# Kernel tuning notes

Measured on AMD Instinct MI355X. Metric: run time of the kernel, lower is better.

Reference implementation:

```python
import jax, jax.numpy as jnp
import numpy as np

N_NODES = 100000
N_EDGES = 1600000
Z_DIM = 64
EDGE_FEAT_DIM = 16
HIDDEN = 128


def setup_inputs() -> dict:
    key = jax.random.key(0)
    k_z, k_ei, k_ea, k_w1, k_b1, k_w2, k_b2 = jax.random.split(key, 7)
    in_dim = 2 * Z_DIM + EDGE_FEAT_DIM
    return {
        "z": jax.random.normal(k_z, (N_NODES, Z_DIM), dtype=jnp.float32),
        "edge_index": jax.random.randint(k_ei, (2, N_EDGES), 0, N_NODES, dtype=jnp.int64),
        "edge_attr": jax.random.normal(k_ea, (N_EDGES, EDGE_FEAT_DIM), dtype=jnp.float32),
        # decoder_mlp params: Linear(2*z_dim+edge_feat_dim, 128) -> ReLU -> Linear(128, 1)
        "W1": jax.random.normal(k_w1, (in_dim, HIDDEN), dtype=jnp.float32) / np.float32(np.sqrt(in_dim)),
        "b1": jax.random.normal(k_b1, (HIDDEN,), dtype=jnp.float32) * 0.01,
        "W2": jax.random.normal(k_w2, (HIDDEN, 1), dtype=jnp.float32) / np.float32(np.sqrt(HIDDEN)),
        "b2": jax.random.normal(k_b2, (1,), dtype=jnp.float32) * 0.01,
    }


def reference(z, edge_index, edge_attr, W1, b1, W2, b2):
    # decode(): gather endpoint embeddings, concat edge features, 2-layer MLP, sigmoid
    src = edge_index[0]
    dst = edge_index[1]
    edge_input = jnp.concatenate([z[src], z[dst], edge_attr], axis=1)  # [E, 2Z+F]
    h = jax.nn.relu(edge_input @ W1 + b1)  # [E, 128]
    logits = h @ W2 + b2                   # [E, 1]
    return jax.nn.sigmoid(logits).squeeze(-1)  # [E]
```

## Files before the change

kernel.cpp:

```cpp
#include <hip/hip_runtime.h>

#define EDGES 1600000
#define NN    100000
#define ZD    64
#define FD    16
#define HID   128
#define BM    32
#define THREADS 256
#define NBLK  1250
#define TPW   10
#define NFRAG 2560
#define WT_SHORTS (NFRAG * 8)

typedef __attribute__((ext_vector_type(8)))  short bfrag;
typedef __attribute__((ext_vector_type(16))) float f16v;

__device__ __forceinline__ unsigned short f2bf(float f) {
  unsigned u = __builtin_bit_cast(unsigned, f);
  u += 0x7fffu + ((u >> 16) & 1u);
  return (unsigned short)(u >> 16);
}
__device__ __forceinline__ unsigned cvtpk(float lo, float hi) {
  unsigned r;
  asm("v_cvt_pk_bf16_f32 %0, %1, %2" : "=v"(r) : "v"(lo), "v"(hi));
  return r;
}
__device__ __forceinline__ void gload16(const void* g, void* l) {
  __builtin_amdgcn_global_load_lds(
      (const __attribute__((address_space(1))) unsigned int*)g,
      (__attribute__((address_space(3))) unsigned int*)l, 16, 0, 0);
}

__global__ void zconv_kernel(const float* __restrict__ z,
                             unsigned short* __restrict__ z16, int n4) {
  int i = blockIdx.x * blockDim.x + threadIdx.x;
  if (i >= n4) return;
  float4 f = reinterpret_cast<const float4*>(z)[i];
  ushort4 p;
  p.x = f2bf(f.x); p.y = f2bf(f.y); p.z = f2bf(f.z); p.w = f2bf(f.w);
  reinterpret_cast<ushort4*>(z16)[i] = p;
}

__global__ void wtab_kernel(const float* __restrict__ W1,
                            const float* __restrict__ b1,
                            unsigned short* __restrict__ WT) {
  int i = blockIdx.x * blockDim.x + threadIdx.x;
  if (i >= WT_SHORTS) return;
  int j    = i & 7;
  int frag = i >> 3;
  int lane = frag & 63;
  int s    = (frag >> 6) % 10;
  int blk  = frag / 640;
  int hid  = blk * 32 + (lane & 31);
  int k    = s * 16 + (lane >> 5) * 8 + j;
  float v = (k < 144) ? W1[k * HID + hid] : (k == 144 ? b1[hid] : 0.f);
  WT[i] = f2bf(v);
}

template<bool ZB>
__global__ __launch_bounds__(THREADS, 2) void fused_kernel(
    const float* __restrict__ zf, const unsigned short* __restrict__ z16,
    const unsigned short* __restrict__ WT,
    const int* __restrict__ ei, const float* __restrict__ ea,
    const float* __restrict__ W2, const float* __restrict__ b2,
    float* __restrict__ out)
{
  __shared__ __align__(16) int4 sW[NFRAG];

  const int tid  = threadIdx.x;
  const int lane = tid & 63;
  const int wid  = tid >> 6;
  const int e    = lane & 31;
  const int hi   = lane >> 5;

  #pragma unroll
  for (int c = 0; c < 10; ++c)
    gload16(WT + (size_t)(c * 256 + tid) * 8, &sW[c * 256 + tid]);
  asm volatile("s_waitcnt vmcnt(0)" ::: "memory");
  __syncthreads();

  float w2v[64];
  #pragma unroll
  for (int blk = 0; blk < 4; ++blk)
    #pragma unroll
    for (int rg = 0; rg < 16; ++rg) {
      int rh = (rg & 3) + 8 * (rg >> 2) + 4 * hi;
      w2v[blk * 16 + rg] = W2[blk * 32 + rh];
    }
  const float bias2 = b2[0];

  int4 oq = {0, 0, 0, 0};
  if (hi == 0) oq.x = 0x3F80;
  const bfrag cone = __builtin_bit_cast(bfrag, oq);

#define GZ(x0, x1, x2, x3, x4, x5, x6, x7, x8, si, di, tt) do {                \
    if constexpr (ZB) {                                                        \
      const unsigned short* ps_ = z16 + (size_t)(si) * ZD + hi * 8;            \
      const unsigned short* pd_ = z16 + (size_t)(di) * ZD + hi * 8;            \
      x0 = *reinterpret_cast<const bfrag*>(ps_);                               \
      x1 = *reinterpret_cast<const bfrag*>(ps_ + 16);                          \
      x2 = *reinterpret_cast<const bfrag*>(ps_ + 32);                          \
      x3 = *reinterpret_cast<const bfrag*>(ps_ + 48);                          \
      x4 = *reinterpret_cast<const bfrag*>(pd_);                               \
      x5 = *reinterpret_cast<const bfrag*>(pd_ + 16);                          \
      x6 = *reinterpret_cast<const bfrag*>(pd_ + 32);                          \
      x7 = *reinterpret_cast<const bfrag*>(pd_ + 48);                          \
    } else {                                                                   \
      const float* ps_ = zf + (size_t)(si) * ZD + hi * 8;                      \
      const float* pd_ = zf + (size_t)(di) * ZD + hi * 8;                      \
      float4 a_, b_;                                                           \
      a_ = ((const float4*)ps_)[0]; b_ = ((const float4*)ps_)[1];              \
      { int4 q_ = {(int)cvtpk(a_.x,a_.y),(int)cvtpk(a_.z,a_.w),                \
                   (int)cvtpk(b_.x,b_.y),(int)cvtpk(b_.z,b_.w)};               \
        x0 = __builtin_bit_cast(bfrag, q_); }                                  \
      a_ = ((const float4*)(ps_+16))[0]; b_ = ((const float4*)(ps_+16))[1];    \
      { int4 q_ = {(int)cvtpk(a_.x,a_.y),(int)cvtpk(a_.z,a_.w),                \
                   (int)cvtpk(b_.x,b_.y),(int)cvtpk(b_.z,b_.w)};               \
        x1 = __builtin_bit_cast(bfrag, q_); }                                  \
      a_ = ((const float4*)(ps_+32))[0]; b_ = ((const float4*)(ps_+32))[1];    \
      { int4 q_ = {(int)cvtpk(a_.x,a_.y),(int)cvtpk(a_.z,a_.w),                \
                   (int)cvtpk(b_.x,b_.y),(int)cvtpk(b_.z,b_.w)};               \
        x2 = __builtin_bit_cast(bfrag, q_); }                                  \
      a_ = ((const float4*)(ps_+48))[0]; b_ = ((const float4*)(ps_+48))[1];    \
      { int4 q_ = {(int)cvtpk(a_.x,a_.y),(int)cvtpk(a_.z,a_.w),                \
                   (int)cvtpk(b_.x,b_.y),(int)cvtpk(b_.z,b_.w)};               \
        x3 = __builtin_bit_cast(bfrag, q_); }                                  \
      a_ = ((const float4*)pd_)[0]; b_ = ((const float4*)pd_)[1];              \
      { int4 q_ = {(int)cvtpk(a_.x,a_.y),(int)cvtpk(a_.z,a_.w),                \
                   (int)cvtpk(b_.x,b_.y),(int)cvtpk(b_.z,b_.w)};               \
        x4 = __builtin_bit_cast(bfrag, q_); }                                  \
      a_ = ((const float4*)(pd_+16))[0]; b_ = ((const float4*)(pd_+16))[1];    \
      { int4 q_ = {(int)cvtpk(a_.x,a_.y),(int)cvtpk(a_.z,a_.w),                \
                   (int)cvtpk(b_.x,b_.y),(int)cvtpk(b_.z,b_.w)};               \
        x5 = __builtin_bit_cast(bfrag, q_); }                                  \
      a_ = ((const float4*)(pd_+32))[0]; b_ = ((const float4*)(pd_+32))[1];    \
      { int4 q_ = {(int)cvtpk(a_.x,a_.y),(int)cvtpk(a_.z,a_.w),                \
                   (int)cvtpk(b_.x,b_.y),(int)cvtpk(b_.z,b_.w)};               \
        x6 = __builtin_bit_cast(bfrag, q_); }                                  \
      a_ = ((const float4*)(pd_+48))[0]; b_ = ((const float4*)(pd_+48))[1];    \
      { int4 q_ = {(int)cvtpk(a_.x,a_.y),(int)cvtpk(a_.z,a_.w),                \
                   (int)cvtpk(b_.x,b_.y),(int)cvtpk(b_.z,b_.w)};               \
        x7 = __builtin_bit_cast(bfrag, q_); }                                  \
    }                                                                          \
    const float* pe_ = ea + ((size_t)(tt) * BM + e) * FD + hi * 8;             \
    float4 ea_ = ((const float4*)pe_)[0];                                      \
    float4 eb_ = ((const float4*)pe_)[1];                                      \
    { int4 q_ = {(int)cvtpk(ea_.x,ea_.y),(int)cvtpk(ea_.z,ea_.w),              \
                 (int)cvtpk(eb_.x,eb_.y),(int)cvtpk(eb_.z,eb_.w)};             \
      x8 = __builtin_bit_cast(bfrag, q_); }                                    \
  } while (0)

  const int gw = blockIdx.x * 4 + wid;
  const int T0 = gw * TPW;

  int si = ei[(size_t)T0 * BM + e];
  int di = ei[(size_t)EDGES + (size_t)T0 * BM + e];
  bfrag c0, c1, c2, c3, c4, c5, c6, c7, c8;
  GZ(c0, c1, c2, c3, c4, c5, c6, c7, c8, si, di, T0);
  int s1 = ei[(size_t)(T0 + 1) * BM + e];
  int d1 = ei[(size_t)EDGES + (size_t)(T0 + 1) * BM + e];

  for (int t = 0; t < TPW; ++t) {
    const int tt = T0 + t;

    const int tn = (t + 1 < TPW) ? tt + 1 : tt;
    bfrag n0, n1, n2, n3, n4, n5, n6, n7, n8;
    GZ(n0, n1, n2, n3, n4, n5, n6, n7, n8, s1, d1, tn);

    const int tf = (t + 2 < TPW) ? tt + 2 : T0 + TPW - 1;
    s1 = ei[(size_t)tf * BM + e];
    d1 = ei[(size_t)EDGES + (size_t)tf * BM + e];

    float p = 0.f;
    #pragma unroll
    for (int blk = 0; blk < 4; ++blk) {
      const int4* wp = &sW[blk * 640 + lane];
      bfrag w0 = *reinterpret_cast<const bfrag*>(wp + 0 * 64);
      bfrag w1 = *reinterpret_cast<const bfrag*>(wp + 1 * 64);
      bfrag w2 = *reinterpret_cast<const bfrag*>(wp + 2 * 64);
      bfrag w3 = *reinterpret_cast<const bfrag*>(wp + 3 * 64);
      bfrag w4 = *reinterpret_cast<const bfrag*>(wp + 4 * 64);
      bfrag w5 = *reinterpret_cast<const bfrag*>(wp + 5 * 64);
      bfrag w6 = *reinterpret_cast<const bfrag*>(wp + 6 * 64);
      bfrag w7 = *reinterpret_cast<const bfrag*>(wp + 7 * 64);
      bfrag w8 = *reinterpret_cast<const bfrag*>(wp + 8 * 64);
      bfrag w9 = *reinterpret_cast<const bfrag*>(wp + 9 * 64);

      f16v acc;
      #pragma unroll
      for (int rg = 0; rg < 16; ++rg) acc[rg] = 0.f;
      acc = __builtin_amdgcn_mfma_f32_32x32x16_bf16(w0, c0, acc, 0, 0, 0);
      acc = __builtin_amdgcn_mfma_f32_32x32x16_bf16(w1, c1, acc, 0, 0, 0);
      acc = __builtin_amdgcn_mfma_f32_32x32x16_bf16(w2, c2, acc, 0, 0, 0);
      acc = __builtin_amdgcn_mfma_f32_32x32x16_bf16(w3, c3, acc, 0, 0, 0);
      acc = __builtin_amdgcn_mfma_f32_32x32x16_bf16(w4, c4, acc, 0, 0, 0);
      acc = __builtin_amdgcn_mfma_f32_32x32x16_bf16(w5, c5, acc, 0, 0, 0);
      acc = __builtin_amdgcn_mfma_f32_32x32x16_bf16(w6, c6, acc, 0, 0, 0);
      acc = __builtin_amdgcn_mfma_f32_32x32x16_bf16(w7, c7, acc, 0, 0, 0);
      acc = __builtin_amdgcn_mfma_f32_32x32x16_bf16(w8, c8, acc, 0, 0, 0);
      acc = __builtin_amdgcn_mfma_f32_32x32x16_bf16(w9, cone, acc, 0, 0, 0);

      #pragma unroll
      for (int rg = 0; rg < 16; ++rg)
        p = fmaf(fmaxf(acc[rg], 0.f), w2v[blk * 16 + rg], p);
    }

    p += __shfl_xor(p, 32);
    if (lane < 32)
      out[(size_t)tt * BM + lane] = 1.f / (1.f + __expf(-(p + bias2)));

    c0 = n0; c1 = n1; c2 = n2; c3 = n3; c4 = n4;
    c5 = n5; c6 = n6; c7 = n7; c8 = n8;
  }
#undef GZ
}

extern "C" void kernel_launch(void* const* d_in, const int* in_sizes, int n_in,
                              void* d_out, int out_size, void* d_ws, size_t ws_size,
                              hipStream_t stream) {
  const float* z  = (const float*)d_in[0];
  const int*   ei = (const int*)d_in[1];
  const float* ea = (const float*)d_in[2];
  const float* W1 = (const float*)d_in[3];
  const float* b1 = (const float*)d_in[4];
  const float* W2 = (const float*)d_in[5];
  const float* b2 = (const float*)d_in[6];
  float* out = (float*)d_out;

  const size_t z16_bytes = (size_t)NN * ZD * sizeof(unsigned short);
  const size_t wt_bytes  = (size_t)WT_SHORTS * sizeof(unsigned short);

  if (ws_size >= z16_bytes + wt_bytes) {
    unsigned short* z16 = (unsigned short*)d_ws;
    unsigned short* WT  = z16 + (size_t)NN * ZD;
    const int n4 = NN * ZD / 4;
    zconv_kernel<<<(n4 + 255) / 256, 256, 0, stream>>>(z, z16, n4);
    wtab_kernel<<<(WT_SHORTS + 255) / 256, 256, 0, stream>>>(W1, b1, WT);
    fused_kernel<true><<<NBLK, THREADS, 0, stream>>>(
        z, z16, WT, ei, ea, W2, b2, out);
  } else {
    unsigned short* WT = (unsigned short*)d_ws;
    wtab_kernel<<<(WT_SHORTS + 255) / 256, 256, 0, stream>>>(W1, b1, WT);
    fused_kernel<false><<<NBLK, THREADS, 0, stream>>>(
        z, nullptr, WT, ei, ea, W2, b2, out);
  }
}
```

Baseline: 99.31 us.

## Split MFMA chain into two accumulators, move W2 to LDS, halve tiles per wave

The single dependent chain of ten MFMAs becomes two independent chains of five, so the matrix unit can interleave them. The partial sums are added before ReLU, and the W2 dot product now uses four accumulators. W2 moves from a 64-float register array into LDS to cut register pressure, and each block now handles half as many tiles, which doubles the block count. In exchange the kernel does an extra vector add per element and more LDS reads, and the per-block weight staging into LDS is repeated twice as often.

```diff
diff --git a/kernel.cpp b/kernel.cpp
--- a/kernel.cpp
+++ b/kernel.cpp
@@ -7,8 +7,8 @@
 #define HID   128
 #define BM    32
 #define THREADS 256
-#define NBLK  1250
-#define TPW   10
+#define NBLK  2500
+#define TPW   5
 #define NFRAG 2560
 #define WT_SHORTS (NFRAG * 8)
 
@@ -66,6 +66,7 @@
     float* __restrict__ out)
 {
   __shared__ __align__(16) int4 sW[NFRAG];
+  __shared__ __align__(16) float sW2[HID];
 
   const int tid  = threadIdx.x;
   const int lane = tid & 63;
@@ -76,22 +77,19 @@
   #pragma unroll
   for (int c = 0; c < 10; ++c)
     gload16(WT + (size_t)(c * 256 + tid) * 8, &sW[c * 256 + tid]);
+  if (tid < HID) sW2[tid] = W2[tid];
   asm volatile("s_waitcnt vmcnt(0)" ::: "memory");
   __syncthreads();
 
-  float w2v[64];
-  #pragma unroll
-  for (int blk = 0; blk < 4; ++blk)
-    #pragma unroll
-    for (int rg = 0; rg < 16; ++rg) {
-      int rh = (rg & 3) + 8 * (rg >> 2) + 4 * hi;
-      w2v[blk * 16 + rg] = W2[blk * 32 + rh];
-    }
   const float bias2 = b2[0];
 
   int4 oq = {0, 0, 0, 0};
   if (hi == 0) oq.x = 0x3F80;
   const bfrag cone = __builtin_bit_cast(bfrag, oq);
+
+  f16v zerov;
+  #pragma unroll
+  for (int rg = 0; rg < 16; ++rg) zerov[rg] = 0.f;
 
 #define GZ(x0, x1, x2, x3, x4, x5, x6, x7, x8, si, di, tt) do {                \
     if constexpr (ZB) {                                                        \
@@ -171,40 +169,60 @@
     s1 = ei[(size_t)tf * BM + e];
     d1 = ei[(size_t)EDGES + (size_t)tf * BM + e];
 
-    float p = 0.f;
+    float p0 = 0.f, p1 = 0.f, p2 = 0.f, p3 = 0.f;
     #pragma unroll
     for (int blk = 0; blk < 4; ++blk) {
       const int4* wp = &sW[blk * 640 + lane];
+
       bfrag w0 = *reinterpret_cast<const bfrag*>(wp + 0 * 64);
+      bfrag w2 = *reinterpret_cast<const bfrag*>(wp + 2 * 64);
+      bfrag w4 = *reinterpret_cast<const bfrag*>(wp + 4 * 64);
+      bfrag w6 = *reinterpret_cast<const bfrag*>(wp + 6 * 64);
+      bfrag w8 = *reinterpret_cast<const bfrag*>(wp + 8 * 64);
+      f16v accA;
+      accA = __builtin_amdgcn_mfma_f32_32x32x16_bf16(w0, c0, zerov, 0, 0, 0);
+      accA = __builtin_amdgcn_mfma_f32_32x32x16_bf16(w2, c2, accA, 0, 0, 0);
+      accA = __builtin_amdgcn_mfma_f32_32x32x16_bf16(w4, c4, accA, 0, 0, 0);
+      accA = __builtin_amdgcn_mfma_f32_32x32x16_bf16(w6, c6, accA, 0, 0, 0);
+      accA = __builtin_amdgcn_mfma_f32_32x32x16_bf16(w8, c8, accA, 0, 0, 0);
+
+      bfrag w9 = *reinterpret_cast<const bfrag*>(wp + 9 * 64);
       bfrag w1 = *reinterpret_cast<const bfrag*>(wp + 1 * 64);
-      bfrag w2 = *reinterpret_cast<const bfrag*>(wp + 2 * 64);
       bfrag w3 = *reinterpret_cast<const bfrag*>(wp + 3 * 64);
-      bfrag w4 = *reinterpret_cast<const bfrag*>(wp + 4 * 64);
       bfrag w5 = *reinterpret_cast<const bfrag*>(wp + 5 * 64);
-      bfrag w6 = *reinterpret_cast<const bfrag*>(wp + 6 * 64);
       bfrag w7 = *reinterpret_cast<const bfrag*>(wp + 7 * 64);
-      bfrag w8 = *reinterpret_cast<const bfrag*>(wp + 8 * 64);
-      bfrag w9 = *reinterpret_cast<const bfrag*>(wp + 9 * 64);
-
-      f16v acc;
-      #pragma unroll
-      for (int rg = 0; rg < 16; ++rg) acc[rg] = 0.f;
-      acc = __builtin_amdgcn_mfma_f32_32x32x16_bf16(w0, c0, acc, 0, 0, 0);
-      acc = __builtin_amdgcn_mfma_f32_32x32x16_bf16(w1, c1, acc, 0, 0, 0);
-      acc = __builtin_amdgcn_mfma_f32_32x32x16_bf16(w2, c2, acc, 0, 0, 0);
-      acc = __builtin_amdgcn_mfma_f32_32x32x16_bf16(w3, c3, acc, 0, 0, 0);
-      acc = __builtin_amdgcn_mfma_f32_32x32x16_bf16(w4, c4, acc, 0, 0, 0);
-      acc = __builtin_amdgcn_mfma_f32_32x32x16_bf16(w5, c5, acc, 0, 0, 0);
-      acc = __builtin_amdgcn_mfma_f32_32x32x16_bf16(w6, c6, acc, 0, 0, 0);
-      acc = __builtin_amdgcn_mfma_f32_32x32x16_bf16(w7, c7, acc, 0, 0, 0);
-      acc = __builtin_amdgcn_mfma_f32_32x32x16_bf16(w8, c8, acc, 0, 0, 0);
-      acc = __builtin_amdgcn_mfma_f32_32x32x16_bf16(w9, cone, acc, 0, 0, 0);
-
-      #pragma unroll
-      for (int rg = 0; rg < 16; ++rg)
-        p = fmaf(fmaxf(acc[rg], 0.f), w2v[blk * 16 + rg], p);
+      f16v accB;
+      accB = __builtin_amdgcn_mfma_f32_32x32x16_bf16(w9, cone, zerov, 0, 0, 0);
+      accB = __builtin_amdgcn_mfma_f32_32x32x16_bf16(w1, c1, accB, 0, 0, 0);
+      accB = __builtin_amdgcn_mfma_f32_32x32x16_bf16(w3, c3, accB, 0, 0, 0);
+      accB = __builtin_amdgcn_mfma_f32_32x32x16_bf16(w5, c5, accB, 0, 0, 0);
+      accB = __builtin_amdgcn_mfma_f32_32x32x16_bf16(w7, c7, accB, 0, 0, 0);
+
+      const float* wq = &sW2[blk * 32 + 4 * hi];
+      float4 q0 = *reinterpret_cast<const float4*>(wq);
+      float4 q1 = *reinterpret_cast<const float4*>(wq + 8);
+      float4 q2 = *reinterpret_cast<const float4*>(wq + 16);
+      float4 q3 = *reinterpret_cast<const float4*>(wq + 24);
+
+      p0 = fmaf(fmaxf(accA[0]  + accB[0],  0.f), q0.x, p0);
+      p1 = fmaf(fmaxf(accA[1]  + accB[1],  0.f), q0.y, p1);
+      p2 = fmaf(fmaxf(accA[2]  + accB[2],  0.f), q0.z, p2);
+      p3 = fmaf(fmaxf(accA[3]  + accB[3],  0.f), q0.w, p3);
+      p0 = fmaf(fmaxf(accA[4]  + accB[4],  0.f), q1.x, p0);
+      p1 = fmaf(fmaxf(accA[5]  + accB[5],  0.f), q1.y, p1);
+      p2 = fmaf(fmaxf(accA[6]  + accB[6],  0.f), q1.z, p2);
+      p3 = fmaf(fmaxf(accA[7]  + accB[7],  0.f), q1.w, p3);
+      p0 = fmaf(fmaxf(accA[8]  + accB[8],  0.f), q2.x, p0);
+      p1 = fmaf(fmaxf(accA[9]  + accB[9],  0.f), q2.y, p1);
+      p2 = fmaf(fmaxf(accA[10] + accB[10], 0.f), q2.z, p2);
+      p3 = fmaf(fmaxf(accA[11] + accB[11], 0.f), q2.w, p3);
+      p0 = fmaf(fmaxf(accA[12] + accB[12], 0.f), q3.x, p0);
+      p1 = fmaf(fmaxf(accA[13] + accB[13], 0.f), q3.y, p1);
+      p2 = fmaf(fmaxf(accA[14] + accB[14], 0.f), q3.z, p2);
+      p3 = fmaf(fmaxf(accA[15] + accB[15], 0.f), q3.w, p3);
     }
 
+    float p = (p0 + p1) + (p2 + p3);
     p += __shfl_xor(p, 32);
     if (lane < 32)
       out[(size_t)tt * BM + lane] = 1.f / (1.f + __expf(-(p + bias2)));
```

New measurement: 107.9 us. 8.7% more time.

## Deepen gather prefetch, split MFMA chains, move W2 to LDS, raise occupancy

Applied to the files above, without the earlier changes.

Each wave now handles 5 tiles instead of 10, with twice as many blocks. The loop is fully unrolled into a triple-buffered schedule that keeps two tiles of gathers in flight ahead of compute. The per-tile MFMA chain is split into two independent accumulators to shorten the dependency chain. W2 moves from 64 per-thread registers into shared memory, freeing registers so launch bounds can ask for 3 blocks per SM. The cost is more LDS reads for W2, more prologue work (the weight-table load into LDS) per edge handled, and register pressure from the three live buffers.

```diff
diff --git a/kernel.cpp b/kernel.cpp
--- a/kernel.cpp
+++ b/kernel.cpp
@@ -7,8 +7,8 @@
 #define HID   128
 #define BM    32
 #define THREADS 256
-#define NBLK  1250
-#define TPW   10
+#define NBLK  2500
+#define TPW   5
 #define NFRAG 2560
 #define WT_SHORTS (NFRAG * 8)
 
@@ -58,7 +58,7 @@
 }
 
 template<bool ZB>
-__global__ __launch_bounds__(THREADS, 2) void fused_kernel(
+__global__ __launch_bounds__(THREADS, 3) void fused_kernel(
     const float* __restrict__ zf, const unsigned short* __restrict__ z16,
     const unsigned short* __restrict__ WT,
     const int* __restrict__ ei, const float* __restrict__ ea,
@@ -66,6 +66,7 @@
     float* __restrict__ out)
 {
   __shared__ __align__(16) int4 sW[NFRAG];
+  __shared__ __align__(16) float sW2[HID];
 
   const int tid  = threadIdx.x;
   const int lane = tid & 63;
@@ -76,24 +77,21 @@
   #pragma unroll
   for (int c = 0; c < 10; ++c)
     gload16(WT + (size_t)(c * 256 + tid) * 8, &sW[c * 256 + tid]);
+  if (tid < HID) sW2[tid] = W2[tid];
   asm volatile("s_waitcnt vmcnt(0)" ::: "memory");
   __syncthreads();
 
-  float w2v[64];
-  #pragma unroll
-  for (int blk = 0; blk < 4; ++blk)
-    #pragma unroll
-    for (int rg = 0; rg < 16; ++rg) {
-      int rh = (rg & 3) + 8 * (rg >> 2) + 4 * hi;
-      w2v[blk * 16 + rg] = W2[blk * 32 + rh];
-    }
   const float bias2 = b2[0];
 
   int4 oq = {0, 0, 0, 0};
   if (hi == 0) oq.x = 0x3F80;
   const bfrag cone = __builtin_bit_cast(bfrag, oq);
 
-#define GZ(x0, x1, x2, x3, x4, x5, x6, x7, x8, si, di, tt) do {                \
+  f16v zerov;
+  #pragma unroll
+  for (int rg = 0; rg < 16; ++rg) zerov[rg] = 0.f;
+
+#define GZ(x0, x1, x2, x3, x4, x5, x6, x7, xa, xb, si, di, tt) do {            \
     if constexpr (ZB) {                                                        \
       const unsigned short* ps_ = z16 + (size_t)(si) * ZD + hi * 8;            \
       const unsigned short* pd_ = z16 + (size_t)(di) * ZD + hi * 8;            \
@@ -143,76 +141,99 @@
         x7 = __builtin_bit_cast(bfrag, q_); }                                  \
     }                                                                          \
     const float* pe_ = ea + ((size_t)(tt) * BM + e) * FD + hi * 8;             \
-    float4 ea_ = ((const float4*)pe_)[0];                                      \
-    float4 eb_ = ((const float4*)pe_)[1];                                      \
-    { int4 q_ = {(int)cvtpk(ea_.x,ea_.y),(int)cvtpk(ea_.z,ea_.w),              \
-                 (int)cvtpk(eb_.x,eb_.y),(int)cvtpk(eb_.z,eb_.w)};             \
-      x8 = __builtin_bit_cast(bfrag, q_); }                                    \
+    xa = ((const float4*)pe_)[0];                                              \
+    xb = ((const float4*)pe_)[1];                                              \
+  } while (0)
+
+#define COMPUTE(x0, x1, x2, x3, x4, x5, x6, x7, xa, xb, tt) do {               \
+    int4 eq_ = {(int)cvtpk(xa.x, xa.y), (int)cvtpk(xa.z, xa.w),                \
+                (int)cvtpk(xb.x, xb.y), (int)cvtpk(xb.z, xb.w)};               \
+    bfrag x8 = __builtin_bit_cast(bfrag, eq_);                                 \
+    float p0 = 0.f, p1 = 0.f, p2 = 0.f, p3 = 0.f;                              \
+    _Pragma("unroll")                                                          \
+    for (int blk = 0; blk < 4; ++blk) {                                        \
+      const int4* wp = &sW[blk * 640 + lane];                                  \
+      bfrag w0 = *reinterpret_cast<const bfrag*>(wp + 0 * 64);                 \
+      bfrag w2 = *reinterpret_cast<const bfrag*>(wp + 2 * 64);                 \
+      bfrag w4 = *reinterpret_cast<const bfrag*>(wp + 4 * 64);                 \
+      bfrag w6 = *reinterpret_cast<const bfrag*>(wp + 6 * 64);                 \
+      bfrag w8 = *reinterpret_cast<const bfrag*>(wp + 8 * 64);                 \
+      f16v accA;                                                               \
+      accA = __builtin_amdgcn_mfma_f32_32x32x16_bf16(w0, x0, zerov, 0, 0, 0);  \
+      accA = __builtin_amdgcn_mfma_f32_32x32x16_bf16(w2, x2, accA, 0, 0, 0);   \
+      accA = __builtin_amdgcn_mfma_f32_32x32x16_bf16(w4, x4, accA, 0, 0, 0);   \
+      accA = __builtin_amdgcn_mfma_f32_32x32x16_bf16(w6, x6, accA, 0, 0, 0);   \
+      accA = __builtin_amdgcn_mfma_f32_32x32x16_bf16(w8, x8, accA, 0, 0, 0);   \
+      bfrag w9 = *reinterpret_cast<const bfrag*>(wp + 9 * 64);                 \
+      bfrag w1 = *reinterpret_cast<const bfrag*>(wp + 1 * 64);                 \
+      bfrag w3 = *reinterpret_cast<const bfrag*>(wp + 3 * 64);                 \
+      bfrag w5 = *reinterpret_cast<const bfrag*>(wp + 5 * 64);                 \
+      bfrag w7 = *reinterpret_cast<const bfrag*>(wp + 7 * 64);                 \
+      f16v accB;                                                               \
+      accB = __builtin_amdgcn_mfma_f32_32x32x16_bf16(w9, cone, zerov, 0, 0, 0);\
+      accB = __builtin_amdgcn_mfma_f32_32x32x16_bf16(w1, x1, accB, 0, 0, 0);   \
+      accB = __builtin_amdgcn_mfma_f32_32x32x16_bf16(w3, x3, accB, 0, 0, 0);   \
+      accB = __builtin_amdgcn_mfma_f32_32x32x16_bf16(w5, x5, accB, 0, 0, 0);   \
+      accB = __builtin_amdgcn_mfma_f32_32x32x16_bf16(w7, x7, accB, 0, 0, 0);   \
+      const float* wq = &sW2[blk * 32 + 4 * hi];                               \
+      float4 q0 = *reinterpret_cast<const float4*>(wq);                        \
+      float4 q1 = *reinterpret_cast<const float4*>(wq + 8);                    \
+      float4 q2 = *reinterpret_cast<const float4*>(wq + 16);                   \
+      float4 q3 = *reinterpret_cast<const float4*>(wq + 24);                   \
+      p0 = fmaf(fmaxf(accA[0]  + accB[0],  0.f), q0.x, p0);                    \
+      p1 = fmaf(fmaxf(accA[1]  + accB[1],  0.f), q0.y, p1);                    \
+      p2 = fmaf(fmaxf(accA[2]  + accB[2],  0.f), q0.z, p2);                    \
+      p3 = fmaf(fmaxf(accA[3]  + accB[3],  0.f), q0.w, p3);                    \
+      p0 = fmaf(fmaxf(accA[4]  + accB[4],  0.f), q1.x, p0);                    \
+      p1 = fmaf(fmaxf(accA[5]  + accB[5],  0.f), q1.y, p1);                    \
+      p2 = fmaf(fmaxf(accA[6]  + accB[6],  0.f), q1.z, p2);                    \
+      p3 = fmaf(fmaxf(accA[7]  + accB[7],  0.f), q1.w, p3);                    \
+      p0 = fmaf(fmaxf(accA[8]  + accB[8],  0.f), q2.x, p0);                    \
+      p1 = fmaf(fmaxf(accA[9]  + accB[9],  0.f), q2.y, p1);                    \
+      p2 = fmaf(fmaxf(accA[10] + accB[10], 0.f), q2.z, p2);                    \
+      p3 = fmaf(fmaxf(accA[11] + accB[11], 0.f), q2.w, p3);                    \
+      p0 = fmaf(fmaxf(accA[12] + accB[12], 0.f), q3.x, p0);                    \
+      p1 = fmaf(fmaxf(accA[13] + accB[13], 0.f), q3.y, p1);                    \
+      p2 = fmaf(fmaxf(accA[14] + accB[14], 0.f), q3.z, p2);                    \
+      p3 = fmaf(fmaxf(accA[15] + accB[15], 0.f), q3.w, p3);                    \
+    }                                                                          \
+    float p = (p0 + p1) + (p2 + p3);                                           \
+    p += __shfl_xor(p, 32);                                                    \
+    if (lane < 32)                                                             \
+      out[(size_t)(tt) * BM + lane] = 1.f / (1.f + __expf(-(p + bias2)));      \
   } while (0)
 
   const int gw = blockIdx.x * 4 + wid;
   const int T0 = gw * TPW;
 
-  int si = ei[(size_t)T0 * BM + e];
-  int di = ei[(size_t)EDGES + (size_t)T0 * BM + e];
-  bfrag c0, c1, c2, c3, c4, c5, c6, c7, c8;
-  GZ(c0, c1, c2, c3, c4, c5, c6, c7, c8, si, di, T0);
-  int s1 = ei[(size_t)(T0 + 1) * BM + e];
-  int d1 = ei[(size_t)EDGES + (size_t)(T0 + 1) * BM + e];
-
-  for (int t = 0; t < TPW; ++t) {
-    const int tt = T0 + t;
-
-    const int tn = (t + 1 < TPW) ? tt + 1 : tt;
-    bfrag n0, n1, n2, n3, n4, n5, n6, n7, n8;
-    GZ(n0, n1, n2, n3, n4, n5, n6, n7, n8, s1, d1, tn);
-
-    const int tf = (t + 2 < TPW) ? tt + 2 : T0 + TPW - 1;
-    s1 = ei[(size_t)tf * BM + e];
-    d1 = ei[(size_t)EDGES + (size_t)tf * BM + e];
-
-    float p = 0.f;
-    #pragma unroll
-    for (int blk = 0; blk < 4; ++blk) {
-      const int4* wp = &sW[blk * 640 + lane];
-      bfrag w0 = *reinterpret_cast<const bfrag*>(wp + 0 * 64);
-      bfrag w1 = *reinterpret_cast<const bfrag*>(wp + 1 * 64);
-      bfrag w2 = *reinterpret_cast<const bfrag*>(wp + 2 * 64);
-      bfrag w3 = *reinterpret_cast<const bfrag*>(wp + 3 * 64);
-      bfrag w4 = *reinterpret_cast<const bfrag*>(wp + 4 * 64);
-      bfrag w5 = *reinterpret_cast<const bfrag*>(wp + 5 * 64);
-      bfrag w6 = *reinterpret_cast<const bfrag*>(wp + 6 * 64);
-      bfrag w7 = *reinterpret_cast<const bfrag*>(wp + 7 * 64);
-      bfrag w8 = *reinterpret_cast<const bfrag*>(wp + 8 * 64);
-      bfrag w9 = *reinterpret_cast<const bfrag*>(wp + 9 * 64);
-
-      f16v acc;
-      #pragma unroll
-      for (int rg = 0; rg < 16; ++rg) acc[rg] = 0.f;
-      acc = __builtin_amdgcn_mfma_f32_32x32x16_bf16(w0, c0, acc, 0, 0, 0);
-      acc = __builtin_amdgcn_mfma_f32_32x32x16_bf16(w1, c1, acc, 0, 0, 0);
-      acc = __builtin_amdgcn_mfma_f32_32x32x16_bf16(w2, c2, acc, 0, 0, 0);
-      acc = __builtin_amdgcn_mfma_f32_32x32x16_bf16(w3, c3, acc, 0, 0, 0);
-      acc = __builtin_amdgcn_mfma_f32_32x32x16_bf16(w4, c4, acc, 0, 0, 0);
-      acc = __builtin_amdgcn_mfma_f32_32x32x16_bf16(w5, c5, acc, 0, 0, 0);
-      acc = __builtin_amdgcn_mfma_f32_32x32x16_bf16(w6, c6, acc, 0, 0, 0);
-      acc = __builtin_amdgcn_mfma_f32_32x32x16_bf16(w7, c7, acc, 0, 0, 0);
-      acc = __builtin_amdgcn_mfma_f32_32x32x16_bf16(w8, c8, acc, 0, 0, 0);
-      acc = __builtin_amdgcn_mfma_f32_32x32x16_bf16(w9, cone, acc, 0, 0, 0);
-
-      #pragma unroll
-      for (int rg = 0; rg < 16; ++rg)
-        p = fmaf(fmaxf(acc[rg], 0.f), w2v[blk * 16 + rg], p);
-    }
-
-    p += __shfl_xor(p, 32);
-    if (lane < 32)
-      out[(size_t)tt * BM + lane] = 1.f / (1.f + __expf(-(p + bias2)));
-
-    c0 = n0; c1 = n1; c2 = n2; c3 = n3; c4 = n4;
-    c5 = n5; c6 = n6; c7 = n7; c8 = n8;
-  }
+  int s0i = ei[(size_t)(T0 + 0) * BM + e], d0i = ei[(size_t)EDGES + (size_t)(T0 + 0) * BM + e];
+  int s1i = ei[(size_t)(T0 + 1) * BM + e], d1i = ei[(size_t)EDGES + (size_t)(T0 + 1) * BM + e];
+  int s2i = ei[(size_t)(T0 + 2) * BM + e], d2i = ei[(size_t)EDGES + (size_t)(T0 + 2) * BM + e];
+  int s3i = ei[(size_t)(T0 + 3) * BM + e], d3i = ei[(size_t)EDGES + (size_t)(T0 + 3) * BM + e];
+
+  bfrag A0, A1, A2, A3, A4, A5, A6, A7; float4 Aa, Ab;
+  bfrag B0, B1, B2, B3, B4, B5, B6, B7; float4 Ba, Bb;
+  bfrag G0, G1, G2, G3, G4, G5, G6, G7; float4 Ga, Gb;
+
+  GZ(A0, A1, A2, A3, A4, A5, A6, A7, Aa, Ab, s0i, d0i, T0 + 0);
+  GZ(B0, B1, B2, B3, B4, B5, B6, B7, Ba, Bb, s1i, d1i, T0 + 1);
+
+  int s4i = ei[(size_t)(T0 + 4) * BM + e], d4i = ei[(size_t)EDGES + (size_t)(T0 + 4) * BM + e];
+  GZ(G0, G1, G2, G3, G4, G5, G6, G7, Ga, Gb, s2i, d2i, T0 + 2);
+  COMPUTE(A0, A1, A2, A3, A4, A5, A6, A7, Aa, Ab, T0 + 0);
+
+  GZ(A0, A1, A2, A3, A4, A5, A6, A7, Aa, Ab, s3i, d3i, T0 + 3);
+  COMPUTE(B0, B1, B2, B3, B4, B5, B6, B7, Ba, Bb, T0 + 1);
+
+  GZ(B0, B1, B2, B3, B4, B5, B6, B7, Ba, Bb, s4i, d4i, T0 + 4);
+  COMPUTE(G0, G1, G2, G3, G4, G5, G6, G7, Ga, Gb, T0 + 2);
+
+  COMPUTE(A0, A1, A2, A3, A4, A5, A6, A7, Aa, Ab, T0 + 3);
+
+  COMPUTE(B0, B1, B2, B3, B4, B5, B6, B7, Ba, Bb, T0 + 4);
+
 #undef GZ
+#undef COMPUTE
 }
 
 extern "C" void kernel_launch(void* const* d_in, const int* in_sizes, int n_in,
```

New measurement: 113.2 us. 14.0% more time.
